# Performance work log

Measured on AMD Instinct MI355X. Metric: run time of the kernel, lower is better.

The kernel has to match this reference:

```python
import jax, jax.numpy as jnp
import numpy as np

Q, K, H, W, D, N, DFF = 48, 48, 24, 8, 512, 3, 2048
S = H * W  # 192
EPS = 1e-5
_BN_SCALE = np.float32(1.0 / np.sqrt(1.0 + EPS))  # eval-mode BN with rm=0, rv=1


def _bn(x, g, b):
    return x * (g * _BN_SCALE) + b


def _layer(tgt, mem, w1, b1, se, g1, bb1, w2, b2, g2, bb2, w3, b3, g3, bb3):
    # tgt: [q, S, D], mem: [k, S, D]
    query = tgt @ w1.T + b1
    key = mem @ w1.T + b1
    gate = jax.nn.sigmoid(se)  # [S, S]
    # large intermediate [q, k, s, t] -- the kernel-headroom hotspot
    score = jnp.einsum('qtd,ksd->qkst', query, key) * gate[None, None]
    qn, kn = tgt.shape[0], mem.shape[0]
    score = score.reshape(qn * kn, S, S)
    # dual max-pool, concatenated as [max_over_s, max_over_t] per pair
    x = jnp.stack([score.max(axis=1), score.max(axis=2)], axis=1).reshape(-1, S)  # [2qk, S]
    x = _bn(x, g1, bb1)
    x = _bn(x @ w2.T + b2, g2, bb2)
    x = jax.nn.relu(x)
    x = x @ w3.T + b3  # [2qk, 1]
    x = x.reshape(-1, 2).sum(axis=-1, keepdims=True)  # [qk, 1]
    x = _bn(x, g3, bb3)
    return x.reshape(qn, kn)


def setup_inputs() -> dict:
    key = jax.random.key(0)
    ks = jax.random.split(key, 16)
    se0 = jax.random.normal(ks[3], (N, S, S), jnp.float32)
    return {
        'memory': jax.random.normal(ks[0], (Q, H, W, D * N), jnp.float32),
        'features': jax.random.normal(ks[1], (K, H, W, D * N), jnp.float32),
        'fc1_w': jax.random.normal(ks[2], (N, D, D), jnp.float32) * np.float32(1.0 / np.sqrt(D)),
        'fc1_b': jnp.zeros((N, D), jnp.float32),
        'score_embed': se0 * np.float32(0.05),
        'bn1_g': 1.0 + 0.1 * jax.random.normal(ks[4], (N,), jnp.float32),
        'bn1_b': 0.1 * jax.random.normal(ks[5], (N,), jnp.float32),
        'fc2_w': jax.random.normal(ks[6], (N, DFF, S), jnp.float32) * np.float32(1.0 / np.sqrt(S)),
        'fc2_b': jnp.zeros((N, DFF), jnp.float32),
        'bn2_g': 1.0 + 0.1 * jax.random.normal(ks[7], (N, DFF), jnp.float32),
        'bn2_b': 0.1 * jax.random.normal(ks[8], (N, DFF), jnp.float32),
        'fc3_w': jax.random.normal(ks[9], (N, 1, DFF), jnp.float32) * np.float32(1.0 / np.sqrt(DFF)),
        'fc3_b': jnp.zeros((N, 1), jnp.float32),
        'bn3_g': 1.0 + 0.1 * jax.random.normal(ks[10], (N,), jnp.float32),
        'bn3_b': 0.1 * jax.random.normal(ks[11], (N,), jnp.float32),
        'norm_g': 1.0 + 0.1 * jax.random.normal(ks[12], (), jnp.float32),
        'norm_b': 0.1 * jax.random.normal(ks[13], (), jnp.float32),
    }


def reference(memory, features, fc1_w, fc1_b, score_embed, bn1_g, bn1_b,
              fc2_w, fc2_b, bn2_g, bn2_b, fc3_w, fc3_b, bn3_g, bn3_b,
              norm_g, norm_b):
    q, k = memory.shape[0], features.shape[0]
    # chunk(dim=-1) into N pieces of width D, then flatten h*w -> S
    tgt = memory.reshape(q, S, N, D)
    mem = features.reshape(k, S, N, D)
    score = jnp.zeros((q, k), jnp.float32)
    for i in range(N):
        score = score + _layer(tgt[:, :, i], mem[:, :, i],
                               fc1_w[i], fc1_b[i], score_embed[i],
                               bn1_g[i], bn1_b[i], fc2_w[i], fc2_b[i],
                               bn2_g[i], bn2_b[i], fc3_w[i], fc3_b[i],
                               bn3_g[i], bn3_b[i])
    # final decoder norm: BatchNorm1d(1) over flattened scores (eval mode)
    score = _bn(score, norm_g, norm_b)
    return score
```

## Files before the change

kernel.cpp:

```cpp
#include <hip/hip_runtime.h>
#include <math.h>

#define BN_SCALE 0.9999950000374997f

typedef unsigned short u16;
typedef short bfrag8 __attribute__((ext_vector_type(8)));
typedef float floatx4 __attribute__((ext_vector_type(4)));

struct ushort4_t { u16 x, y, z, w; };

__device__ __forceinline__ u16 f2bf(float f) {
  union { float f; unsigned u; } c; c.f = f;
  unsigned r = c.u + 0x7FFFu + ((c.u >> 16) & 1u);
  return (u16)(r >> 16);
}

__device__ __forceinline__ void gload_lds16(const u16* g, u16* l) {
  __builtin_amdgcn_global_load_lds(
      (const __attribute__((address_space(1))) void*)g,
      (__attribute__((address_space(3))) void*)l, 16, 0, 0);
}

__device__ __forceinline__ floatx4 mfma16(bfrag8 a, bfrag8 b, floatx4 c) {
  return __builtin_amdgcn_mfma_f32_16x16x32_bf16(a, b, c, 0, 0, 0);
}

__global__ void k_gate(const float* __restrict__ se, float* __restrict__ gate) {
  int idx = blockIdx.x * 256 + threadIdx.x;
  if (idx < 3 * 192 * 192) {
    float x = se[idx];
    gate[idx] = 1.0f / (1.0f + expf(-x));
  }
}

__global__ __launch_bounds__(256, 1) void k_fc1(
    const float* __restrict__ memin, const float* __restrict__ featin,
    const float* __restrict__ w1, const float* __restrict__ b1,
    u16* __restrict__ qB, u16* __restrict__ kB) {
  __shared__ u16 At[128 * 64];
  __shared__ u16 Bt[128 * 64];
  const int tid = threadIdx.x, lane = tid & 63, wave = tid >> 6;
  const int bz = blockIdx.z, n = bz >> 1, side = bz & 1;
  const int m0 = blockIdx.y * 128, n0 = blockIdx.x * 128;
  const float* A = (side ? featin : memin) + n * 512;
  const float* B = w1 + (size_t)n * 512 * 512;
  u16* C = (side ? kB : qB) + (size_t)n * 9216 * 512;

  floatx4 acc[4][4];
  for (int i = 0; i < 4; i++)
    for (int j = 0; j < 4; j++) acc[i][j] = (floatx4){0.f, 0.f, 0.f, 0.f};
  const int wr = wave >> 1, wc = wave & 1;
  const int lr = lane & 15, lq = lane >> 4;

  for (int kk = 0; kk < 8; ++kk) {
    const int k0 = kk * 64;
    __syncthreads();
    for (int it = 0; it < 8; ++it) {
      int s = it * 256 + tid;
      int row = s >> 4, c4 = (s & 15) << 2;
      float4 av = *(const float4*)&A[(size_t)(m0 + row) * 1536 + k0 + c4];
      ushort4_t ah = {f2bf(av.x), f2bf(av.y), f2bf(av.z), f2bf(av.w)};
      *(ushort4_t*)&At[row * 64 + c4] = ah;
      float4 bv = *(const float4*)&B[(size_t)(n0 + row) * 512 + k0 + c4];
      ushort4_t bh = {f2bf(bv.x), f2bf(bv.y), f2bf(bv.z), f2bf(bv.w)};
      *(ushort4_t*)&Bt[row * 64 + c4] = bh;
    }
    __syncthreads();
    for (int k2 = 0; k2 < 64; k2 += 32) {
      bfrag8 a[4], b[4];
      for (int i = 0; i < 4; i++)
        a[i] = *(const bfrag8*)&At[(wr * 64 + i * 16 + lr) * 64 + k2 + lq * 8];
      for (int j = 0; j < 4; j++)
        b[j] = *(const bfrag8*)&Bt[(wc * 64 + j * 16 + lr) * 64 + k2 + lq * 8];
      for (int i = 0; i < 4; i++)
        for (int j = 0; j < 4; j++) acc[i][j] = mfma16(a[i], b[j], acc[i][j]);
    }
  }
  for (int j = 0; j < 4; j++) {
    int col = n0 + wc * 64 + j * 16 + lr;
    float bias = b1[n * 512 + col];
    int ct = col >> 6, cw = col & 63;
    for (int i = 0; i < 4; i++) {
      int rbase = m0 + wr * 64 + i * 16 + lq * 4;
      for (int rg = 0; rg < 4; rg++) {
        int rr = rbase + rg;
        int tile = rr / 192, rw = rr - tile * 192;
        C[(size_t)tile * (192 * 512) + ct * (192 * 64) + rw * 64 + cw] =
            f2bf(acc[i][j][rg] + bias);
      }
    }
  }
}

__global__ __launch_bounds__(256, 2) void k_score(
    const u16* __restrict__ qB, const u16* __restrict__ kB,
    const float* __restrict__ gate,
    const float* __restrict__ bn1g, const float* __restrict__ bn1b,
    u16* __restrict__ pooled) {
  __shared__ __align__(16) u16 At[192 * 64];
  __shared__ __align__(16) u16 Bt[192 * 64];
  const int tid = threadIdx.x, lane = tid & 63, wave = tid >> 6;
  const int lin = blockIdx.x, n = blockIdx.y;
  const int xcd = lin & 7, idx = lin >> 3;
  const int qIdx = idx / 6, kIdx = xcd * 6 + (idx - (idx / 6) * 6);
  const u16* A = kB + (size_t)n * 9216 * 512 + (size_t)kIdx * (192 * 512);
  const u16* Bp = qB + (size_t)n * 9216 * 512 + (size_t)qIdx * (192 * 512);
  const int ws = wave >> 1, wt = wave & 1;
  const int lr = lane & 15, lq = lane >> 4;
  const int sw = lr & 7;
  const int cc0 = (lq ^ sw) << 3;
  const int cc1 = ((lq + 4) ^ sw) << 3;

  floatx4 acc[6][6];
  for (int i = 0; i < 6; i++)
    for (int j = 0; j < 6; j++) acc[i][j] = (floatx4){0.f, 0.f, 0.f, 0.f};

  for (int kk = 0; kk < 8; ++kk) {
    const u16* Akk = A + kk * (192 * 64);
    const u16* Bkk = Bp + kk * (192 * 64);
    __syncthreads();
    for (int it = 0; it < 6; ++it) {
      int chb = it * 256 + wave * 64;
      int ch = chb + lane;
      int row = ch >> 3, cc = ch & 7;
      int src = (row << 3) + (cc ^ (row & 7));
      gload_lds16(Akk + src * 8, &At[chb * 8]);
      gload_lds16(Bkk + src * 8, &Bt[chb * 8]);
    }
    __syncthreads();
#pragma unroll
    for (int k2 = 0; k2 < 2; ++k2) {
      const int cco = k2 ? cc1 : cc0;
      bfrag8 a[6], b[6];
      for (int i = 0; i < 6; i++)
        a[i] = *(const bfrag8*)&At[(ws * 96 + i * 16 + lr) * 64 + cco];
      for (int j = 0; j < 6; j++)
        b[j] = *(const bfrag8*)&Bt[(wt * 96 + j * 16 + lr) * 64 + cco];
      for (int i = 0; i < 6; i++)
        for (int j = 0; j < 6; j++) acc[i][j] = mfma16(a[i], b[j], acc[i][j]);
    }
  }

  const float* gaten = gate + (size_t)n * 36864;
  float colp[6], rowp[6][4];
  for (int j = 0; j < 6; j++) colp[j] = -INFINITY;
  for (int i = 0; i < 6; i++)
    for (int rg = 0; rg < 4; rg++) rowp[i][rg] = -INFINITY;
  for (int i = 0; i < 6; i++) {
    for (int j = 0; j < 6; j++) {
      int t = wt * 96 + j * 16 + lr;
      for (int rg = 0; rg < 4; rg++) {
        int s = ws * 96 + i * 16 + lq * 4 + rg;
        float v = acc[i][j][rg] * gaten[s * 192 + t];
        colp[j] = fmaxf(colp[j], v);
        rowp[i][rg] = fmaxf(rowp[i][rg], v);
      }
    }
  }
  __syncthreads();
  float* colL = (float*)At;
  float* rowL = (float*)Bt;
  for (int j = 0; j < 6; j++)
    colL[(ws * 4 + lq) * 192 + wt * 96 + j * 16 + lr] = colp[j];
  for (int i = 0; i < 6; i++)
    for (int rg = 0; rg < 4; rg++) {
      float v = rowp[i][rg];
      v = fmaxf(v, __shfl_xor(v, 1));
      v = fmaxf(v, __shfl_xor(v, 2));
      v = fmaxf(v, __shfl_xor(v, 4));
      v = fmaxf(v, __shfl_xor(v, 8));
      if (lr == 0) rowL[wt * 192 + ws * 96 + i * 16 + lq * 4 + rg] = v;
    }
  __syncthreads();

  const float g1 = bn1g[n] * BN_SCALE;
  const float bb1 = bn1b[n];
  u16* outp = pooled + ((size_t)n * 2304 + (size_t)qIdx * 48 + kIdx) * 384;
  for (int id = tid; id < 384; id += 256) {
    if (id < 192) {
      float m = colL[id];
      for (int w = 1; w < 8; w++) m = fmaxf(m, colL[w * 192 + id]);
      outp[id] = f2bf(m * g1 + bb1);
    } else {
      int s = id - 192;
      float m = fmaxf(rowL[s], rowL[192 + s]);
      outp[id] = f2bf(m * g1 + bb1);
    }
  }
}

__global__ __launch_bounds__(256, 1) void k_mlp(
    const u16* __restrict__ pooled, const float* __restrict__ w2,
    const float* __restrict__ b2, const float* __restrict__ g2,
    const float* __restrict__ bb2, const float* __restrict__ w3,
    float* __restrict__ r) {
  __shared__ u16 Xt[128 * 64];
  __shared__ u16 Wt[128 * 64];
  const int tid = threadIdx.x, lane = tid & 63, wave = tid >> 6;
  const int n = blockIdx.z, row0 = blockIdx.y * 128, f0 = blockIdx.x * 512;
  const u16* X = pooled + ((size_t)n * 4608 + row0) * 192;
  const float* W = w2 + (size_t)n * 2048 * 192;
  const int wr = wave >> 1, wc = wave & 1;
  const int lr = lane & 15, lq = lane >> 4;
  float rp[4][4];
  for (int i = 0; i < 4; i++)
    for (int rg = 0; rg < 4; rg++) rp[i][rg] = 0.f;

  for (int fs = 0; fs < 4; ++fs) {
    const int fb = f0 + fs * 128;
    floatx4 acc[4][4];
    for (int i = 0; i < 4; i++)
      for (int j = 0; j < 4; j++) acc[i][j] = (floatx4){0.f, 0.f, 0.f, 0.f};
    for (int kk = 0; kk < 3; ++kk) {
      const int k0 = kk * 64;
      __syncthreads();
      for (int it = 0; it < 4; ++it) {
        int sb = (wave * 4 + it) * 64;
        int s = sb + lane;
        int row = s >> 3, c8 = (s & 7) << 3;
        gload_lds16(X + (size_t)row * 192 + k0 + c8, &Xt[sb * 8]);
      }
      for (int it = 0; it < 8; ++it) {
        int s = it * 256 + tid;
        int row = s >> 4, c4 = (s & 15) << 2;
        float4 wv = *(const float4*)&W[(size_t)(fb + row) * 192 + k0 + c4];
        ushort4_t wh = {f2bf(wv.x), f2bf(wv.y), f2bf(wv.z), f2bf(wv.w)};
        *(ushort4_t*)&Wt[row * 64 + c4] = wh;
      }
      __syncthreads();
      for (int k2 = 0; k2 < 64; k2 += 32) {
        bfrag8 a[4], b[4];
        for (int i = 0; i < 4; i++)
          a[i] = *(const bfrag8*)&Xt[(wr * 64 + i * 16 + lr) * 64 + k2 + lq * 8];
        for (int j = 0; j < 4; j++)
          b[j] = *(const bfrag8*)&Wt[(wc * 64 + j * 16 + lr) * 64 + k2 + lq * 8];
        for (int i = 0; i < 4; i++)
          for (int j = 0; j < 4; j++) acc[i][j] = mfma16(a[i], b[j], acc[i][j]);
      }
    }
    for (int j = 0; j < 4; j++) {
      int f = fb + wc * 64 + j * 16 + lr;
      float alpha = g2[n * 2048 + f] * BN_SCALE;
      float beta = b2[n * 2048 + f] * alpha + bb2[n * 2048 + f];
      float w3f = w3[n * 2048 + f];
      for (int i = 0; i < 4; i++)
        for (int rg = 0; rg < 4; rg++) {
          float y = acc[i][j][rg] * alpha + beta;
          y = fmaxf(y, 0.f);
          rp[i][rg] += y * w3f;
        }
    }
  }
  for (int i = 0; i < 4; i++)
    for (int rg = 0; rg < 4; rg++) {
      float v = rp[i][rg];
      v += __shfl_xor(v, 1);
      v += __shfl_xor(v, 2);
      v += __shfl_xor(v, 4);
      v += __shfl_xor(v, 8);
      if (lr == 0) {
        int row = row0 + wr * 64 + i * 16 + lq * 4 + rg;
        atomicAdd(&r[n * 4608 + row], v);
      }
    }
}

__global__ void k_final(const float* __restrict__ r, const float* __restrict__ b3,
                        const float* __restrict__ g3, const float* __restrict__ bb3,
                        const float* __restrict__ ng, const float* __restrict__ nb,
                        float* __restrict__ out) {
  int p = blockIdx.x * 256 + threadIdx.x;
  if (p >= 2304) return;
  float acc = 0.f;
  for (int n = 0; n < 3; ++n) {
    float z = r[n * 4608 + 2 * p] + r[n * 4608 + 2 * p + 1] + 2.f * b3[n];
    acc += z * (g3[n] * BN_SCALE) + bb3[n];
  }
  out[p] = acc * (ng[0] * BN_SCALE) + nb[0];
}

extern "C" void kernel_launch(void* const* d_in, const int* in_sizes, int n_in,
                              void* d_out, int out_size, void* d_ws, size_t ws_size,
                              hipStream_t stream) {
  const float* memory = (const float*)d_in[0];
  const float* features = (const float*)d_in[1];
  const float* fc1_w = (const float*)d_in[2];
  const float* fc1_b = (const float*)d_in[3];
  const float* se = (const float*)d_in[4];
  const float* bn1_g = (const float*)d_in[5];
  const float* bn1_b = (const float*)d_in[6];
  const float* fc2_w = (const float*)d_in[7];
  const float* fc2_b = (const float*)d_in[8];
  const float* bn2_g = (const float*)d_in[9];
  const float* bn2_b = (const float*)d_in[10];
  const float* fc3_w = (const float*)d_in[11];
  const float* fc3_b = (const float*)d_in[12];
  const float* bn3_g = (const float*)d_in[13];
  const float* bn3_b = (const float*)d_in[14];
  const float* norm_g = (const float*)d_in[15];
  const float* norm_b = (const float*)d_in[16];

  char* ws = (char*)d_ws;
  float* gate = (float*)ws;
  u16* qB = (u16*)(ws + 442368);
  u16* kB = (u16*)(ws + 442368 + 28311552);
  u16* pooled = (u16*)(ws + 442368 + 2 * 28311552);
  float* r = (float*)(ws + 442368 + 2 * 28311552 + 5308416);

  hipMemsetAsync(r, 0, 3 * 4608 * sizeof(float), stream);
  k_gate<<<dim3(432), 256, 0, stream>>>(se, gate);
  k_fc1<<<dim3(4, 72, 6), 256, 0, stream>>>(memory, features, fc1_w, fc1_b, qB, kB);
  k_score<<<dim3(2304, 3), 256, 0, stream>>>(qB, kB, gate, bn1_g, bn1_b, pooled);
  k_mlp<<<dim3(4, 36, 3), 256, 0, stream>>>(pooled, fc2_w, fc2_b, bn2_g, bn2_b, fc3_w, r);
  k_final<<<dim3(9), 256, 0, stream>>>(r, fc3_b, bn3_g, bn3_b, norm_g, norm_b,
                                       (float*)d_out);
}
```

Baseline: 541.5 us.

## Pre-swizzle q/k into MFMA fragment layout and drop LDS staging in score kernel

fc1 now writes its query/key outputs directly in the per-lane MFMA fragment order, so the score kernel loads its fragments straight from global memory into registers with no LDS staging and no barriers in the main loop. A new prep kernel also converts fc2 weights once to bf16 with the BN2 scale folded in and precomputes the bias, so the MLP kernel can load weights with direct-to-LDS copies and an XOR swizzle. The tradeoff is that the score kernel no longer shares tiles through LDS, so each wave reads its operands from global/L2 separately, which raises cache traffic and puts more latency on the load path.

```diff
diff --git a/kernel.cpp b/kernel.cpp
--- a/kernel.cpp
+++ b/kernel.cpp
@@ -25,12 +25,25 @@
   return __builtin_amdgcn_mfma_f32_16x16x32_bf16(a, b, c, 0, 0, 0);
 }
 
-__global__ void k_gate(const float* __restrict__ se, float* __restrict__ gate) {
+
+__global__ void k_prep(const float* __restrict__ se, float* __restrict__ gate,
+                       const float* __restrict__ w2, const float* __restrict__ g2,
+                       const float* __restrict__ b2, const float* __restrict__ bb2,
+                       u16* __restrict__ w2B, float* __restrict__ beta2) {
   int idx = blockIdx.x * 256 + threadIdx.x;
-  if (idx < 3 * 192 * 192) {
+  if (idx < 110592) {
     float x = se[idx];
     gate[idx] = 1.0f / (1.0f + expf(-x));
-  }
+    return;
+  }
+  idx -= 110592;
+  if (idx < 1179648) {
+    int nf = idx / 192;
+    w2B[idx] = f2bf(w2[idx] * (g2[nf] * BN_SCALE));
+    return;
+  }
+  idx -= 1179648;
+  if (idx < 6144) beta2[idx] = b2[idx] * (g2[idx] * BN_SCALE) + bb2[idx];
 }
 
 __global__ __launch_bounds__(256, 1) void k_fc1(
@@ -44,7 +57,7 @@
   const int m0 = blockIdx.y * 128, n0 = blockIdx.x * 128;
   const float* A = (side ? featin : memin) + n * 512;
   const float* B = w1 + (size_t)n * 512 * 512;
-  u16* C = (side ? kB : qB) + (size_t)n * 9216 * 512;
+  u16* Cn = (side ? kB : qB) + (size_t)n * 4718592;
 
   floatx4 acc[4][4];
   for (int i = 0; i < 4; i++)
@@ -79,13 +92,15 @@
   for (int j = 0; j < 4; j++) {
     int col = n0 + wc * 64 + j * 16 + lr;
     float bias = b1[n * 512 + col];
-    int ct = col >> 6, cw = col & 63;
+    int kc = col >> 5;
+    int lq2 = (col >> 3) & 3, e = col & 7;
     for (int i = 0; i < 4; i++) {
       int rbase = m0 + wr * 64 + i * 16 + lq * 4;
       for (int rg = 0; rg < 4; rg++) {
         int rr = rbase + rg;
         int tile = rr / 192, rw = rr - tile * 192;
-        C[(size_t)tile * (192 * 512) + ct * (192 * 64) + rw * 64 + cw] =
+        int rb = rw >> 4, lrD = rw & 15;
+        Cn[(((size_t)tile * 16 + kc) * 12 + rb) * 512 + (lq2 * 16 + lrD) * 8 + e] =
             f2bf(acc[i][j][rg] + bias);
       }
     }
@@ -97,48 +112,35 @@
     const float* __restrict__ gate,
     const float* __restrict__ bn1g, const float* __restrict__ bn1b,
     u16* __restrict__ pooled) {
-  __shared__ __align__(16) u16 At[192 * 64];
-  __shared__ __align__(16) u16 Bt[192 * 64];
+  __shared__ float colL[8 * 192];
+  __shared__ float rowL[2 * 192];
   const int tid = threadIdx.x, lane = tid & 63, wave = tid >> 6;
   const int lin = blockIdx.x, n = blockIdx.y;
   const int xcd = lin & 7, idx = lin >> 3;
   const int qIdx = idx / 6, kIdx = xcd * 6 + (idx - (idx / 6) * 6);
-  const u16* A = kB + (size_t)n * 9216 * 512 + (size_t)kIdx * (192 * 512);
-  const u16* Bp = qB + (size_t)n * 9216 * 512 + (size_t)qIdx * (192 * 512);
   const int ws = wave >> 1, wt = wave & 1;
   const int lr = lane & 15, lq = lane >> 4;
-  const int sw = lr & 7;
-  const int cc0 = (lq ^ sw) << 3;
-  const int cc1 = ((lq + 4) ^ sw) << 3;
+
+  const u16* Ap = kB + (((size_t)(n * 48 + kIdx) * 16) * 12 + ws * 6) * 512 + lane * 8;
+  const u16* Bp = qB + (((size_t)(n * 48 + qIdx) * 16) * 12 + wt * 6) * 512 + lane * 8;
 
   floatx4 acc[6][6];
   for (int i = 0; i < 6; i++)
     for (int j = 0; j < 6; j++) acc[i][j] = (floatx4){0.f, 0.f, 0.f, 0.f};
 
-  for (int kk = 0; kk < 8; ++kk) {
-    const u16* Akk = A + kk * (192 * 64);
-    const u16* Bkk = Bp + kk * (192 * 64);
-    __syncthreads();
-    for (int it = 0; it < 6; ++it) {
-      int chb = it * 256 + wave * 64;
-      int ch = chb + lane;
-      int row = ch >> 3, cc = ch & 7;
-      int src = (row << 3) + (cc ^ (row & 7));
-      gload_lds16(Akk + src * 8, &At[chb * 8]);
-      gload_lds16(Bkk + src * 8, &Bt[chb * 8]);
-    }
-    __syncthreads();
-#pragma unroll
-    for (int k2 = 0; k2 < 2; ++k2) {
-      const int cco = k2 ? cc1 : cc0;
-      bfrag8 a[6], b[6];
-      for (int i = 0; i < 6; i++)
-        a[i] = *(const bfrag8*)&At[(ws * 96 + i * 16 + lr) * 64 + cco];
-      for (int j = 0; j < 6; j++)
-        b[j] = *(const bfrag8*)&Bt[(wt * 96 + j * 16 + lr) * 64 + cco];
-      for (int i = 0; i < 6; i++)
-        for (int j = 0; j < 6; j++) acc[i][j] = mfma16(a[i], b[j], acc[i][j]);
-    }
+#pragma unroll 4
+  for (int kc = 0; kc < 16; ++kc) {
+    bfrag8 a[6], b[6];
+#pragma unroll
+    for (int i = 0; i < 6; i++) a[i] = *(const bfrag8*)(Ap + i * 512);
+#pragma unroll
+    for (int j = 0; j < 6; j++) b[j] = *(const bfrag8*)(Bp + j * 512);
+#pragma unroll
+    for (int i = 0; i < 6; i++)
+#pragma unroll
+      for (int j = 0; j < 6; j++) acc[i][j] = mfma16(a[i], b[j], acc[i][j]);
+    Ap += 6144;
+    Bp += 6144;
   }
 
   const float* gaten = gate + (size_t)n * 36864;
@@ -157,9 +159,6 @@
       }
     }
   }
-  __syncthreads();
-  float* colL = (float*)At;
-  float* rowL = (float*)Bt;
   for (int j = 0; j < 6; j++)
     colL[(ws * 4 + lq) * 192 + wt * 96 + j * 16 + lr] = colp[j];
   for (int i = 0; i < 6; i++)
@@ -190,18 +189,19 @@
 }
 
 __global__ __launch_bounds__(256, 1) void k_mlp(
-    const u16* __restrict__ pooled, const float* __restrict__ w2,
-    const float* __restrict__ b2, const float* __restrict__ g2,
-    const float* __restrict__ bb2, const float* __restrict__ w3,
+    const u16* __restrict__ pooled, const u16* __restrict__ w2B,
+    const float* __restrict__ beta2, const float* __restrict__ w3,
     float* __restrict__ r) {
   __shared__ u16 Xt[128 * 64];
   __shared__ u16 Wt[128 * 64];
   const int tid = threadIdx.x, lane = tid & 63, wave = tid >> 6;
   const int n = blockIdx.z, row0 = blockIdx.y * 128, f0 = blockIdx.x * 512;
   const u16* X = pooled + ((size_t)n * 4608 + row0) * 192;
-  const float* W = w2 + (size_t)n * 2048 * 192;
+  const u16* W = w2B + (size_t)n * 2048 * 192;
   const int wr = wave >> 1, wc = wave & 1;
   const int lr = lane & 15, lq = lane >> 4;
+  const int sw = lr & 7;
+  const int cc0 = (lq ^ sw) << 3, cc1 = ((lq + 4) ^ sw) << 3;
   float rp[4][4];
   for (int i = 0; i < 4; i++)
     for (int rg = 0; rg < 4; rg++) rp[i][rg] = 0.f;
@@ -215,37 +215,33 @@
       const int k0 = kk * 64;
       __syncthreads();
       for (int it = 0; it < 4; ++it) {
-        int sb = (wave * 4 + it) * 64;
-        int s = sb + lane;
-        int row = s >> 3, c8 = (s & 7) << 3;
-        gload_lds16(X + (size_t)row * 192 + k0 + c8, &Xt[sb * 8]);
-      }
-      for (int it = 0; it < 8; ++it) {
-        int s = it * 256 + tid;
-        int row = s >> 4, c4 = (s & 15) << 2;
-        float4 wv = *(const float4*)&W[(size_t)(fb + row) * 192 + k0 + c4];
-        ushort4_t wh = {f2bf(wv.x), f2bf(wv.y), f2bf(wv.z), f2bf(wv.w)};
-        *(ushort4_t*)&Wt[row * 64 + c4] = wh;
+        int chb = it * 256 + wave * 64;
+        int ch = chb + lane;
+        int row = ch >> 3, cc = ch & 7;
+        int scc = ((cc ^ (row & 7)) << 3);
+        gload_lds16(X + (size_t)row * 192 + k0 + scc, &Xt[chb * 8]);
+        gload_lds16(W + (size_t)(fb + row) * 192 + k0 + scc, &Wt[chb * 8]);
       }
       __syncthreads();
-      for (int k2 = 0; k2 < 64; k2 += 32) {
+#pragma unroll
+      for (int k2 = 0; k2 < 2; ++k2) {
+        const int cco = k2 ? cc1 : cc0;
         bfrag8 a[4], b[4];
         for (int i = 0; i < 4; i++)
-          a[i] = *(const bfrag8*)&Xt[(wr * 64 + i * 16 + lr) * 64 + k2 + lq * 8];
+          a[i] = *(const bfrag8*)&Xt[(wr * 64 + i * 16 + lr) * 64 + cco];
         for (int j = 0; j < 4; j++)
-          b[j] = *(const bfrag8*)&Wt[(wc * 64 + j * 16 + lr) * 64 + k2 + lq * 8];
+          b[j] = *(const bfrag8*)&Wt[(wc * 64 + j * 16 + lr) * 64 + cco];
         for (int i = 0; i < 4; i++)
           for (int j = 0; j < 4; j++) acc[i][j] = mfma16(a[i], b[j], acc[i][j]);
       }
     }
     for (int j = 0; j < 4; j++) {
       int f = fb + wc * 64 + j * 16 + lr;
-      float alpha = g2[n * 2048 + f] * BN_SCALE;
-      float beta = b2[n * 2048 + f] * alpha + bb2[n * 2048 + f];
+      float beta = beta2[n * 2048 + f];
       float w3f = w3[n * 2048 + f];
       for (int i = 0; i < 4; i++)
         for (int rg = 0; rg < 4; rg++) {
-          float y = acc[i][j][rg] * alpha + beta;
+          float y = acc[i][j][rg] + beta;
           y = fmaxf(y, 0.f);
           rp[i][rg] += y * w3f;
         }
@@ -302,16 +298,19 @@
 
   char* ws = (char*)d_ws;
   float* gate = (float*)ws;
-  u16* qB = (u16*)(ws + 442368);
-  u16* kB = (u16*)(ws + 442368 + 28311552);
-  u16* pooled = (u16*)(ws + 442368 + 2 * 28311552);
-  float* r = (float*)(ws + 442368 + 2 * 28311552 + 5308416);
+  u16* w2B = (u16*)(ws + 442368);
+  float* beta2 = (float*)(ws + 2801664);
+  u16* qB = (u16*)(ws + 2826240);
+  u16* kB = (u16*)(ws + 31137792);
+  u16* pooled = (u16*)(ws + 59449344);
+  float* r = (float*)(ws + 64757760);
 
   hipMemsetAsync(r, 0, 3 * 4608 * sizeof(float), stream);
-  k_gate<<<dim3(432), 256, 0, stream>>>(se, gate);
+  k_prep<<<dim3(5064), 256, 0, stream>>>(se, gate, fc2_w, bn2_g, fc2_b, bn2_b,
+                                         w2B, beta2);
   k_fc1<<<dim3(4, 72, 6), 256, 0, stream>>>(memory, features, fc1_w, fc1_b, qB, kB);
   k_score<<<dim3(2304, 3), 256, 0, stream>>>(qB, kB, gate, bn1_g, bn1_b, pooled);
-  k_mlp<<<dim3(4, 36, 3), 256, 0, stream>>>(pooled, fc2_w, fc2_b, bn2_g, bn2_b, fc3_w, r);
+  k_mlp<<<dim3(4, 36, 3), 256, 0, stream>>>(pooled, w2B, beta2, fc3_w, r);
   k_final<<<dim3(9), 256, 0, stream>>>(r, fc3_b, bn3_g, bn3_b, norm_g, norm_b,
                                        (float*)d_out);
 }
```

Result: slower. 683.1 us (+26.1%).
